# Performance work log

Hardware: AMD Instinct MI355X
Metric: run time of the kernel (lower is better)

The kernel has to match this reference:

```python
import jax, jax.numpy as jnp
import numpy as np

B, S, D, H = 8, 512, 1024, 16
DH = D // H
GAMMA = 0.1      # kl_gamma
KL_EPS = 1e-10
LN_EPS = 1e-5
SCALE = 1.0 / np.sqrt(DH).astype(np.float32)


def setup_inputs() -> dict:
    key = jax.random.key(0)
    ks = iter(jax.random.split(key, 32))
    rnd = lambda shape, s: jax.random.normal(next(ks), shape, jnp.float32) * s
    inp = {
        'title_features': rnd((B, S, D), 1.0),
        'content_features': rnd((B, S, D), 1.0),
    }
    for pre in ('t2c', 'c2t'):
        # small Q/K weights + bias 1.0 keep row-means of scores positive (log is defined)
        inp[pre + '_wq'] = rnd((D, D), 0.02); inp[pre + '_bq'] = jnp.ones((D,), jnp.float32)
        inp[pre + '_wk'] = rnd((D, D), 0.02); inp[pre + '_bk'] = jnp.ones((D,), jnp.float32)
        inp[pre + '_wv'] = rnd((D, D), 0.02); inp[pre + '_bv'] = jnp.zeros((D,), jnp.float32)
        inp[pre + '_wo'] = rnd((D, D), 0.02); inp[pre + '_bo'] = jnp.zeros((D,), jnp.float32)
    inp['gate_w'] = rnd((2 * D, D), 0.02)
    inp['gate_b'] = jnp.zeros((D,), jnp.float32)
    inp['ln_g'] = jnp.ones((D,), jnp.float32)
    inp['ln_b'] = jnpps = jnp.zeros((D,), jnp.float32)
    inp['ln_b'] = jnp.zeros((D,), jnp.float32)
    return inp


def _daa(q_in, k_in, v_in, wq, bq, wk, bk, wv, bv, wo, bo):
    """DivergenceAlignedAttention forward (eval mode, use_uniform_target=False)."""
    Bq, Sq, _ = q_in.shape
    Sk = k_in.shape[1]
    Q = (q_in @ wq + bq).reshape(Bq, Sq, H, DH)
    K = (k_in @ wk + bk).reshape(Bq, Sk, H, DH)
    V = (v_in @ wv + bv).reshape(Bq, Sk, H, DH)
    scores = jnp.einsum('bqhd,bkhd->bhqk', Q, K) * SCALE           # [B,H,Sq,Sk]
    tgt = jnp.mean(scores, axis=-1, keepdims=True)                 # row mean
    scores = scores + GAMMA * jnp.log(tgt + KL_EPS)                # fused KL term
    attn = jax.nn.softmax(scores, axis=-1)
    ctx = jnp.einsum('bhqk,bkhd->bqhd', attn, V).reshape(Bq, Sq, D)
    return ctx @ wo + bo


def _layer_norm(x, g, b):
    mu = jnp.mean(x, axis=-1, keepdims=True)
    var = jnp.mean(jnp.square(x - mu), axis=-1, keepdims=True)
    return g * (x - mu) / jnp.sqrt(var + LN_EPS) + b


def reference(title_features, content_features,
              t2c_wq, t2c_bq, t2c_wk, t2c_bk, t2c_wv, t2c_bv, t2c_wo, t2c_bo,
              c2t_wq, c2t_bq, c2t_wk, c2t_bk, c2t_wv, c2t_bv, c2t_wo, c2t_bo,
              gate_w, gate_b, ln_g, ln_b):
    t2c = _daa(content_features, title_features, title_features,
               t2c_wq, t2c_bq, t2c_wk, t2c_bk, t2c_wv, t2c_bv, t2c_wo, t2c_bo)
    c2t = _daa(title_features, content_features, content_features,
               c2t_wq, c2t_bq, c2t_wk, c2t_bk, c2t_wv, c2t_bv, c2t_wo, c2t_bo)
    gate_t = jax.nn.sigmoid(jnp.concatenate([title_features, t2c], axis=-1) @ gate_w + gate_b)
    gate_c = jax.nn.sigmoid(jnp.concatenate([content_features, c2t], axis=-1) @ gate_w + gate_b)
    fused_title = _layer_norm(gate_t * title_features + (1.0 - gate_t) * t2c, ln_g, ln_b)
    fused_content = _layer_norm(gate_c * content_features + (1.0 - gate_c) * c2t, ln_g, ln_b)
    return (fused_title, fused_content)
```

## Files before the change

### kernel.cpp

```cpp
#include <hip/hip_runtime.h>
#include <cstdint>
#include <cstddef>

typedef unsigned short ushort_t;
typedef unsigned int u32;
typedef __attribute__((ext_vector_type(8))) short bf16x8;
typedef __attribute__((ext_vector_type(4))) float f32x4;
typedef __attribute__((ext_vector_type(4))) unsigned short u16x4;

#define DEV static __device__ __forceinline__

DEV ushort_t f2bf(float f) {
  u32 x = __float_as_uint(f);
  x += 0x7fff + ((x >> 16) & 1);
  return (ushort_t)(x >> 16);
}
DEV float bf2f(ushort_t u) { return __uint_as_float(((u32)u) << 16); }

DEV void gload16(const ushort_t* g, ushort_t* l) {
  __builtin_amdgcn_global_load_lds(
      (const __attribute__((address_space(1))) void*)g,
      (__attribute__((address_space(3))) void*)l, 16, 0, 0);
}


__global__ __launch_bounds__(256) void cvt_inputs(
    const float* __restrict__ xa, const float* __restrict__ xb,
    ushort_t* __restrict__ oa, ushort_t* __restrict__ ob) {
  int i = blockIdx.x * 256 + threadIdx.x;
  f32x4 va = ((const f32x4*)xa)[i];
  f32x4 vb = ((const f32x4*)xb)[i];
  u16x4 ua, ub;
#pragma unroll
  for (int j = 0; j < 4; ++j) { ua[j] = f2bf(va[j]); ub[j] = f2bf(vb[j]); }
  ((u16x4*)oa)[i] = ua;
  ((u16x4*)ob)[i] = ub;
}

struct Src11 { const float* p[11]; };

__global__ __launch_bounds__(256) void transpose_cvt(
    Src11 srcs, ushort_t* __restrict__ WTall, ushort_t* __restrict__ WgT,
    ushort_t* __restrict__ WoBF) {
  const int z = blockIdx.z;
  if (z != 8 && blockIdx.y >= 32) return;
  const float* src = srcs.p[z];
  int tx = threadIdx.x & 31, ty = threadIdx.x >> 5;
  int n0 = blockIdx.x << 5, k0 = blockIdx.y << 5;
  if (z >= 9) {
    ushort_t* dst = WoBF + ((size_t)(z - 9) << 20);
#pragma unroll
    for (int i = 0; i < 4; ++i) {
      size_t off = (size_t)(k0 + ty + i * 8) * 1024 + n0 + tx;
      dst[off] = f2bf(src[off]);
    }
    return;
  }
  const int K = (z == 8) ? 2048 : 1024;
  ushort_t* dst = (z == 8) ? WgT : WTall + ((size_t)z << 20);
  __shared__ float t[32][33];
#pragma unroll
  for (int i = 0; i < 4; ++i)
    t[ty + i * 8][tx] = src[(size_t)(k0 + ty + i * 8) * 1024 + n0 + tx];
  __syncthreads();
#pragma unroll
  for (int i = 0; i < 4; ++i)
    dst[(size_t)(n0 + ty + i * 8) * K + k0 + tx] = f2bf(t[tx][ty + i * 8]);
}

__global__ __launch_bounds__(256) void gb2_kernel(
    const float* __restrict__ bo0, const float* __restrict__ bo1,
    const ushort_t* __restrict__ WgT, float* __restrict__ gb2) {
  const int wgl = blockIdx.x * 4 + (threadIdx.x >> 6);
  const int lane = threadIdx.x & 63;
  const int dir = wgl >> 10, n = wgl & 1023;
  const float* bo = dir ? bo1 : bo0;
  const ushort_t* wrow = WgT + ((size_t)n << 11) + 1024 + (lane << 4);
  float s = 0.f;
#pragma unroll
  for (int j = 0; j < 16; ++j) s += bo[(lane << 4) + j] * bf2f(wrow[j]);
#pragma unroll
  for (int d = 1; d < 64; d <<= 1) s += __shfl_xor(s, d, 64);
  if (lane == 0) gb2[wgl] = s;
}

__global__ __launch_bounds__(256, 3) void gemm_wp(
    const ushort_t* __restrict__ WgT, const ushort_t* __restrict__ WoBF,
    ushort_t* __restrict__ WpT) {
  __shared__ ushort_t As[128 * 64];
  __shared__ ushort_t Bs[128 * 64];
  const int tid = threadIdx.x;
  const int w = tid >> 6, lane = tid & 63;
  const int g = lane >> 4, c = lane & 15;
  const int wm = (w >> 1) << 6, wn = (w & 1) << 6;
  const int m0 = blockIdx.x << 7, n0 = blockIdx.y << 7;
  const int group = m0 >> 10;
  const int csw = (lane & 7) ^ (lane >> 3);

  f32x4 acc[4][4];
#pragma unroll
  for (int i = 0; i < 4; ++i)
#pragma unroll
    for (int j = 0; j < 4; ++j) acc[i][j] = f32x4{0.f, 0.f, 0.f, 0.f};

  for (int k0 = 0; k0 < 1024; k0 += 64) {
#pragma unroll
    for (int i = 0; i < 4; ++i) {
      const int chunk = (w << 2) + i;
      const int row = (chunk << 3) + (lane >> 3);
      gload16(WgT + ((size_t)((m0 + row) & 1023) << 11) + 1024 + k0 + (csw << 3),
              &As[(size_t)chunk << 9]);
      gload16(WoBF + ((size_t)group << 20) + ((size_t)(n0 + row) << 10) + k0 + (csw << 3),
              &Bs[(size_t)chunk << 9]);
    }
    __syncthreads();
    const int cg = c & 7;
#pragma unroll
    for (int ks = 0; ks < 2; ++ks) {
      bf16x8 af[4], bfr[4];
#pragma unroll
      for (int mi = 0; mi < 4; ++mi)
        af[mi] = *(const bf16x8*)&As[((wm + mi * 16 + c) << 6) +
                                     ((((ks << 2) | g) ^ cg) << 3)];
#pragma unroll
      for (int ni = 0; ni < 4; ++ni)
        bfr[ni] = *(const bf16x8*)&Bs[((wn + ni * 16 + c) << 6) +
                                      ((((ks << 2) | g) ^ cg) << 3)];
#pragma unroll
      for (int mi = 0; mi < 4; ++mi)
#pragma unroll
        for (int ni = 0; ni < 4; ++ni)
          acc[mi][ni] = __builtin_amdgcn_mfma_f32_16x16x32_bf16(
              af[mi], bfr[ni], acc[mi][ni], 0, 0, 0);
    }
    __syncthreads();
  }
#pragma unroll
  for (int ni = 0; ni < 4; ++ni) {
    const int n = n0 + wn + ni * 16 + c;
#pragma unroll
    for (int mi = 0; mi < 4; ++mi) {
      const int mb = m0 + wm + mi * 16 + (g << 2);
      f32x4 a = acc[mi][ni];
#pragma unroll
      for (int r = 0; r < 4; ++r)
        WpT[((size_t)group << 20) + ((size_t)((mb + r) & 1023) << 10) + n] = f2bf(a[r]);
    }
  }
}

enum { M_QKVG = 0, M_OG = 1 };
struct Bias8 { const float* p[8]; };

template <int MODE>
__global__ __launch_bounds__(256, 3) void gemm_kernel(
    const ushort_t* __restrict__ Aa, const ushort_t* __restrict__ Ab,
    const ushort_t* __restrict__ WTall, const ushort_t* __restrict__ WgT,
    const ushort_t* __restrict__ WpT, Bias8 bt, const float* __restrict__ gb2,
    ushort_t* __restrict__ outQ, ushort_t* __restrict__ gt) {
  __shared__ ushort_t As[128 * 64];
  __shared__ ushort_t Bs[128 * 64];
  const int tid = threadIdx.x;
  const int w = tid >> 6, lane = tid & 63;
  const int g = lane >> 4, c = lane & 15;
  const int wm = (w >> 1) << 6, wn = (w & 1) << 6;
  const int bid = (int)blockIdx.x;
  const int xcd = bid & 7, idx = bid >> 3;
  const int mt = (xcd << 3) + (idx & 7), nt = idx >> 3;
  const int m0 = mt << 7, n0 = nt << 7;
  const int group = m0 >> 12;
  const int nch = n0 >> 10;
  const int csw = (lane & 7) ^ (lane >> 3);

  const ushort_t* Asrc = (MODE == M_QKVG)
      ? ((group ? Ab : Aa) + ((size_t)(m0 & 4095) << 10))
      : (Aa + ((size_t)m0 << 10));

  const ushort_t* Bb;
  int bstr, bidx = -1;
  if (MODE == M_QKVG) {
    if (nch < 3) {
      bidx = group * 3 + nch;
      Bb = WTall + ((size_t)bidx << 20) + ((size_t)(n0 & 1023) << 10);
      bstr = 1024;
    } else {
      Bb = WgT + ((size_t)(n0 & 1023) << 11);
      bstr = 2048;
    }
  } else {
    if (nch == 0) {
      Bb = WTall + ((size_t)(6 + group) << 20) + ((size_t)n0 << 10);
      bstr = 1024;
    } else {
      Bb = WpT + ((size_t)group << 20) + ((size_t)(n0 & 1023) << 10);
      bstr = 1024;
    }
  }

  f32x4 acc[4][4];
#pragma unroll
  for (int i = 0; i < 4; ++i)
#pragma unroll
    for (int j = 0; j < 4; ++j) acc[i][j] = f32x4{0.f, 0.f, 0.f, 0.f};

  for (int k0 = 0; k0 < 1024; k0 += 64) {
#pragma unroll
    for (int i = 0; i < 4; ++i) {
      const int chunk = (w << 2) + i;
      const int row = (chunk << 3) + (lane >> 3);
      gload16(Asrc + ((size_t)row << 10) + k0 + (csw << 3), &As[(size_t)chunk << 9]);
      gload16(Bb + (size_t)row * bstr + k0 + (csw << 3), &Bs[(size_t)chunk << 9]);
    }
    __syncthreads();
    const int cg = c & 7;
#pragma unroll
    for (int ks = 0; ks < 2; ++ks) {
      bf16x8 af[4], bfr[4];
#pragma unroll
      for (int mi = 0; mi < 4; ++mi)
        af[mi] = *(const bf16x8*)&As[((wm + mi * 16 + c) << 6) +
                                     ((((ks << 2) | g) ^ cg) << 3)];
#pragma unroll
      for (int ni = 0; ni < 4; ++ni)
        bfr[ni] = *(const bf16x8*)&Bs[((wn + ni * 16 + c) << 6) +
                                      ((((ks << 2) | g) ^ cg) << 3)];
#pragma unroll
      for (int mi = 0; mi < 4; ++mi)
#pragma unroll
        for (int ni = 0; ni < 4; ++ni)
          acc[mi][ni] = __builtin_amdgcn_mfma_f32_16x16x32_bf16(
              af[mi], bfr[ni], acc[mi][ni], 0, 0, 0);
    }
    __syncthreads();
  }

#pragma unroll
  for (int ni = 0; ni < 4; ++ni) {
    const int n = n0 + wn + ni * 16 + c;
    const int nloc = n & 1023;
    float bv;
    if (MODE == M_QKVG)
      bv = (nch < 3) ? bt.p[bidx][nloc]
                     : bt.p[6][nloc] + gb2[(group << 10) + nloc];
    else
      bv = (nch == 0) ? bt.p[group][nloc] : 0.f;
#pragma unroll
    for (int mi = 0; mi < 4; ++mi) {
      const int mb = m0 + wm + mi * 16 + (g << 2);
      f32x4 a = acc[mi][ni];
      if (MODE == M_QKVG) {
        if (nch < 3) {
          const int mrow = mb & 4095, b = mrow >> 9, s = mrow & 511;
          const int h = nloc >> 6, d = nloc & 63;
          ushort_t* base = outQ + ((size_t)bidx << 22);
          if (bidx == 1 || bidx == 5) {
            u16x4 o;
#pragma unroll
            for (int r = 0; r < 4; ++r) o[r] = f2bf(a[r] + bv);
            *(u16x4*)&base[(((size_t)((b * 16 + h) * 64 + d)) << 9) + s] = o;
          } else {
#pragma unroll
            for (int r = 0; r < 4; ++r)
              base[(((size_t)((b * 16 + h) * 512 + s + r)) << 6) + d] = f2bf(a[r] + bv);
          }
        } else {
#pragma unroll
          for (int r = 0; r < 4; ++r)
            gt[((size_t)(mb + r) << 10) + nloc] = f2bf(a[r] + bv);
        }
      } else {
        if (nch == 0) {
#pragma unroll
          for (int r = 0; r < 4; ++r)
            outQ[((size_t)(mb + r) << 10) + nloc] = f2bf(a[r] + bv);
        } else {
#pragma unroll
          for (int r = 0; r < 4; ++r)
            gt[((size_t)(mb + r) << 10) + nloc] = f2bf(a[r]);
        }
      }
    }
  }
}

__global__ __launch_bounds__(256, 4) void attn_kernel(
    const ushort_t* __restrict__ QKV, ushort_t* __restrict__ ctx) {
  __shared__ ushort_t Ks[2][4096];
  __shared__ ushort_t Vs[2][4096];
  const int tid = threadIdx.x, w = tid >> 6, lane = tid & 63;
  const int g = lane >> 4, c = lane & 15, c7 = c & 7;
  const int bid = (int)blockIdx.x;
  const int wid = (bid & 7) * 256 + (bid >> 3);
  const int dir = wid >> 10;
  const int bh = (wid >> 3) & 127, qt = wid & 7;
  const int q0 = (qt << 6) + (w << 4);
  const int qs = dir ? 2 : 3, ks = dir ? 4 : 0, vs = dir ? 5 : 1;
  const ushort_t* Qb = QKV + ((size_t)qs << 22) + ((size_t)bh << 15);
  const ushort_t* Kb = QKV + ((size_t)ks << 22) + ((size_t)bh << 15);
  const ushort_t* Vb = QKV + ((size_t)vs << 22) + ((size_t)bh << 15);

  auto stageK = [&](int b, int kc) {
#pragma unroll
    for (int i = 0; i < 2; ++i) {
      int idx = tid + (i << 8);
      int r = idx >> 3, sl = idx & 7;
      int cs = sl ^ (r & 7);
      gload16(Kb + (((size_t)((kc << 6) + r)) << 6) + (cs << 3), &Ks[b][idx << 3]);
    }
  };
  auto stageV = [&](int b, int vc) {
#pragma unroll
    for (int i = 0; i < 2; ++i) {
      int idx = tid + (i << 8);
      int r = idx >> 3, sl = idx & 7;
      int cs = sl ^ (r & 7);
      gload16(Vb + ((size_t)r << 9) + (vc << 6) + (cs << 3), &Vs[b][idx << 3]);
    }
  };

  bf16x8 qf0 = *(const bf16x8*)&Qb[((q0 + c) << 6) + (g << 3)];
  bf16x8 qf1 = *(const bf16x8*)&Qb[((q0 + c) << 6) + 32 + (g << 3)];

  const float SC = 0.125f;
  float m = -1e30f, sum = 0.f;
  f32x4 pacc[4];
#pragma unroll
  for (int dt = 0; dt < 4; ++dt) pacc[dt] = f32x4{0.f, 0.f, 0.f, 0.f};
  const int s1 = ((g & 1) << 5) + c;
  const int s2 = s1 + 16;
  const bool hi = (g >> 1) != 0;

  stageK(0, 0);
  stageV(0, 0);
  __syncthreads();

#pragma unroll
  for (int cc = 0; cc < 8; ++cc) {
    const int buf = cc & 1;
    if (cc < 7) { stageK(buf ^ 1, cc + 1); stageV(buf ^ 1, cc + 1); }

    f32x4 st[4];
    __builtin_amdgcn_s_setprio(1);
#pragma unroll
    for (int t = 0; t < 4; ++t) {
      const ushort_t* base = &Ks[buf][((t << 4) + c) << 6];
      bf16x8 a0 = *(const bf16x8*)&base[(g ^ c7) << 3];
      bf16x8 a1 = *(const bf16x8*)&base[((4 | g) ^ c7) << 3];
      f32x4 z = {0.f, 0.f, 0.f, 0.f};
      z = __builtin_amdgcn_mfma_f32_16x16x32_bf16(a0, qf0, z, 0, 0, 0);
      z = __builtin_amdgcn_mfma_f32_16x16x32_bf16(a1, qf1, z, 0, 0, 0);
      st[t] = z;
    }
    __builtin_amdgcn_s_setprio(0);

    float mx = fmaxf(fmaxf(st[0][0], st[0][1]), fmaxf(st[0][2], st[0][3]));
#pragma unroll
    for (int t = 1; t < 4; ++t)
      mx = fmaxf(mx, fmaxf(fmaxf(st[t][0], st[t][1]), fmaxf(st[t][2], st[t][3])));
    mx = fmaxf(mx, __shfl_xor(mx, 16, 64));
    mx = fmaxf(mx, __shfl_xor(mx, 32, 64));
    const float mn = fmaxf(m, mx);
    const float scale = __expf((m - mn) * SC);
    m = mn;
    float ls = 0.f;
#pragma unroll
    for (int t = 0; t < 4; ++t)
#pragma unroll
      for (int r = 0; r < 4; ++r) {
        float p = __expf((st[t][r] - mn) * SC);
        st[t][r] = p;
        ls += p;
      }
    ls += __shfl_xor(ls, 16, 64);
    ls += __shfl_xor(ls, 32, 64);
    sum = sum * scale + ls;
#pragma unroll
    for (int dt = 0; dt < 4; ++dt)
#pragma unroll
      for (int r = 0; r < 4; ++r) pacc[dt][r] *= scale;

#pragma unroll
    for (int u = 0; u < 2; ++u) {
      u32 A0 = ((u32)f2bf(st[2 * u][1]) << 16) | f2bf(st[2 * u][0]);
      u32 A1p = ((u32)f2bf(st[2 * u][3]) << 16) | f2bf(st[2 * u][2]);
      u32 B0 = ((u32)f2bf(st[2 * u + 1][1]) << 16) | f2bf(st[2 * u + 1][0]);
      u32 B1 = ((u32)f2bf(st[2 * u + 1][3]) << 16) | f2bf(st[2 * u + 1][2]);
      u32 xA0 = (u32)__shfl((int)A0, s1, 64), xA1 = (u32)__shfl((int)A1p, s1, 64);
      u32 xB0 = (u32)__shfl((int)B0, s1, 64), xB1 = (u32)__shfl((int)B1, s1, 64);
      u32 yA0 = (u32)__shfl((int)A0, s2, 64), yA1 = (u32)__shfl((int)A1p, s2, 64);
      u32 yB0 = (u32)__shfl((int)B0, s2, 64), yB1 = (u32)__shfl((int)B1, s2, 64);
      union { bf16x8 v; u32 wd[4]; } pb;
      pb.wd[0] = hi ? xB0 : xA0;
      pb.wd[1] = hi ? xB1 : xA1;
      pb.wd[2] = hi ? yB0 : yA0;
      pb.wd[3] = hi ? yB1 : yA1;
      __builtin_amdgcn_s_setprio(1);
#pragma unroll
      for (int dt = 0; dt < 4; ++dt) {
        bf16x8 av = *(const bf16x8*)
            &Vs[buf][(((dt << 4) + c) << 6) + ((((u << 2) | g) ^ c7) << 3)];
        pacc[dt] = __builtin_amdgcn_mfma_f32_16x16x32_bf16(av, pb.v, pacc[dt], 0, 0, 0);
      }
      __builtin_amdgcn_s_setprio(0);
    }
    __syncthreads();
  }

  const float inv = 1.0f / sum;
  const int b = bh >> 4, h = bh & 15;
  size_t obase = ((size_t)dir << 22) + ((size_t)(b * 512 + q0 + c) << 10) + (h << 6);
#pragma unroll
  for (int dt = 0; dt < 4; ++dt) {
    u16x4 o;
#pragma unroll
    for (int r = 0; r < 4; ++r) o[r] = f2bf(pacc[dt][r] * inv);
    *(u16x4*)&ctx[obase + (dt << 4) + (g << 2)] = o;
  }
}

__global__ __launch_bounds__(256) void fuse_ln(
    const float* __restrict__ xt, const float* __restrict__ xc,
    const ushort_t* __restrict__ ao, const ushort_t* __restrict__ gt,
    const ushort_t* __restrict__ gp,
    const float* __restrict__ lng, const float* __restrict__ lnb,
    float* __restrict__ out) {
  const int row = blockIdx.x, dir = row >> 12, r = row & 4095;
  const float* x = (dir ? xc : xt) + ((size_t)r << 10);
  const ushort_t* a = ao + ((size_t)row << 10);
  const ushort_t* g1 = gt + ((size_t)row << 10);
  const ushort_t* g2 = gp + ((size_t)row << 10);
  float* o = out + ((size_t)row << 10);
  const int t = threadIdx.x, w = t >> 6, lane = t & 63;
  f32x4 xv = ((const f32x4*)x)[t];
  u16x4 av = ((const u16x4*)a)[t];
  u16x4 gv = ((const u16x4*)g1)[t];
  u16x4 pv = ((const u16x4*)g2)[t];
  f32x4 f;
  float sm = 0.f, sq = 0.f;
#pragma unroll
  for (int j = 0; j < 4; ++j) {
    float gate = 1.f / (1.f + __expf(-(bf2f(gv[j]) + bf2f(pv[j]))));
    float fv = gate * xv[j] + (1.f - gate) * bf2f(av[j]);
    f[j] = fv; sm += fv; sq += fv * fv;
  }
#pragma unroll
  for (int d = 1; d < 64; d <<= 1) {
    sm += __shfl_xor(sm, d, 64);
    sq += __shfl_xor(sq, d, 64);
  }
  __shared__ float ps[8];
  if (lane == 0) { ps[w] = sm; ps[4 + w] = sq; }
  __syncthreads();
  sm = ps[0] + ps[1] + ps[2] + ps[3];
  sq = ps[4] + ps[5] + ps[6] + ps[7];
  const float mu = sm * (1.f / 1024.f);
  const float var = sq * (1.f / 1024.f) - mu * mu;
  const float rstd = rsqrtf(var + 1e-5f);
  f32x4 lg = ((const f32x4*)lng)[t], lb = ((const f32x4*)lnb)[t];
  f32x4 ov;
#pragma unroll
  for (int j = 0; j < 4; ++j) ov[j] = lg[j] * (f[j] - mu) * rstd + lb[j];
  ((f32x4*)o)[t] = ov;
}

extern "C" void kernel_launch(void* const* d_in, const int* in_sizes, int n_in,
                              void* d_out, int out_size, void* d_ws, size_t ws_size,
                              hipStream_t stream) {
  (void)in_sizes; (void)n_in; (void)out_size; (void)ws_size;
  const float* title = (const float*)d_in[0];
  const float* content = (const float*)d_in[1];

  char* ws = (char*)d_ws;
  const size_t MB = 1u << 20;
  ushort_t* Xt    = (ushort_t*)(ws + 0 * MB);
  ushort_t* Xc    = (ushort_t*)(ws + 8 * MB);
  ushort_t* ctx   = (ushort_t*)(ws + 0 * MB);
  ushort_t* WTall = (ushort_t*)(ws + 16 * MB);
  ushort_t* WgT   = (ushort_t*)(ws + 32 * MB);
  ushort_t* QKV   = (ushort_t*)(ws + 36 * MB);
  ushort_t* ao    = (ushort_t*)(ws + 36 * MB);
  ushort_t* gpart = (ushort_t*)(ws + 52 * MB);
  ushort_t* gt    = (ushort_t*)(ws + 84 * MB);
  ushort_t* WoBF  = (ushort_t*)(ws + 100 * MB);
  ushort_t* WpT   = (ushort_t*)(ws + 104 * MB);
  float*    gb2   = (float*)   (ws + 108 * MB);

  cvt_inputs<<<4096, 256, 0, stream>>>(title, content, Xt, Xc);

  Src11 srcs;
  srcs.p[0] = (const float*)d_in[4];  srcs.p[1] = (const float*)d_in[6];
  srcs.p[2] = (const float*)d_in[10]; srcs.p[3] = (const float*)d_in[2];
  srcs.p[4] = (const float*)d_in[12]; srcs.p[5] = (const float*)d_in[14];
  srcs.p[6] = (const float*)d_in[8];  srcs.p[7] = (const float*)d_in[16];
  srcs.p[8] = (const float*)d_in[18];
  srcs.p[9] = (const float*)d_in[8];  srcs.p[10] = (const float*)d_in[16];
  transpose_cvt<<<dim3(32, 64, 11), 256, 0, stream>>>(srcs, WTall, WgT, WoBF);

  gb2_kernel<<<512, 256, 0, stream>>>((const float*)d_in[9], (const float*)d_in[17],
                                      WgT, gb2);
  gemm_wp<<<dim3(16, 8), 256, 0, stream>>>(WgT, WoBF, WpT);

  Bias8 bq;
  bq.p[0] = (const float*)d_in[5];  bq.p[1] = (const float*)d_in[7];
  bq.p[2] = (const float*)d_in[11]; bq.p[3] = (const float*)d_in[3];
  bq.p[4] = (const float*)d_in[13]; bq.p[5] = (const float*)d_in[15];
  bq.p[6] = (const float*)d_in[19]; bq.p[7] = nullptr;
  gemm_kernel<M_QKVG><<<2048, 256, 0, stream>>>(Xt, Xc, WTall, WgT, WpT, bq, gb2,
                                                QKV, gt);

  attn_kernel<<<2048, 256, 0, stream>>>(QKV, ctx);

  Bias8 bo;
  bo.p[0] = (const float*)d_in[9]; bo.p[1] = (const float*)d_in[17];
  for (int i = 2; i < 8; ++i) bo.p[i] = nullptr;
  gemm_kernel<M_OG><<<1024, 256, 0, stream>>>(ctx, nullptr, WTall, WgT, WpT, bo, gb2,
                                              ao, gpart);

  fuse_ln<<<8192, 256, 0, stream>>>(title, content, ao, gt, gpart,
                                    (const float*)d_in[20], (const float*)d_in[21],
                                    (float*)d_out);
}
```

Measured before the change: 224.3 us.

## Double-buffer GEMM K-loop and store Q/K row-major instead of head-major

The GEMM main loop now uses two 128x32 LDS buffers per operand and prefetches the next K slice while running MFMAs on the current one. This replaces the single-buffer load/sync/compute pattern and raises MFMA priority. Q and K projections are now written in plain [B*S, D] row-major layout rather than head-major, and the attention kernel indexes them with a 1024-element row stride. This keeps the GEMM epilogue stores contiguous, at the cost of strided per-head reads in attention and twice as many barriers per K step.

Result: slower. 245.0 us (+9.2%).

```diff
diff --git a/kernel.cpp b/kernel.cpp
--- a/kernel.cpp
+++ b/kernel.cpp
@@ -158,8 +158,8 @@
     const ushort_t* __restrict__ WTall, const ushort_t* __restrict__ WgT,
     const ushort_t* __restrict__ WpT, Bias8 bt, const float* __restrict__ gb2,
     ushort_t* __restrict__ outQ, ushort_t* __restrict__ gt) {
-  __shared__ ushort_t As[128 * 64];
-  __shared__ ushort_t Bs[128 * 64];
+  __shared__ ushort_t As[2][128 * 32];
+  __shared__ ushort_t Bs[2][128 * 32];
   const int tid = threadIdx.x;
   const int w = tid >> 6, lane = tid & 63;
   const int g = lane >> 4, c = lane & 15;
@@ -170,7 +170,6 @@
   const int m0 = mt << 7, n0 = nt << 7;
   const int group = m0 >> 12;
   const int nch = n0 >> 10;
-  const int csw = (lane & 7) ^ (lane >> 3);
 
   const ushort_t* Asrc = (MODE == M_QKVG)
       ? ((group ? Ab : Aa) + ((size_t)(m0 & 4095) << 10))
@@ -197,40 +196,48 @@
     }
   }
 
+  auto stage = [&](int bf_, int k0) {
+#pragma unroll
+    for (int j = 0; j < 2; ++j) {
+      const int blkc = (w << 1) + j;
+      const int row = (blkc << 4) + (lane >> 2);
+      const int cs = (lane & 3) ^ ((row >> 1) & 3);
+      gload16(Asrc + ((size_t)row << 10) + k0 + (cs << 3), &As[bf_][blkc << 9]);
+      gload16(Bb + (size_t)row * bstr + k0 + (cs << 3), &Bs[bf_][blkc << 9]);
+    }
+  };
+
   f32x4 acc[4][4];
 #pragma unroll
   for (int i = 0; i < 4; ++i)
 #pragma unroll
     for (int j = 0; j < 4; ++j) acc[i][j] = f32x4{0.f, 0.f, 0.f, 0.f};
 
-  for (int k0 = 0; k0 < 1024; k0 += 64) {
-#pragma unroll
-    for (int i = 0; i < 4; ++i) {
-      const int chunk = (w << 2) + i;
-      const int row = (chunk << 3) + (lane >> 3);
-      gload16(Asrc + ((size_t)row << 10) + k0 + (csw << 3), &As[(size_t)chunk << 9]);
-      gload16(Bb + (size_t)row * bstr + k0 + (csw << 3), &Bs[(size_t)chunk << 9]);
-    }
-    __syncthreads();
-    const int cg = c & 7;
-#pragma unroll
-    for (int ks = 0; ks < 2; ++ks) {
-      bf16x8 af[4], bfr[4];
-#pragma unroll
-      for (int mi = 0; mi < 4; ++mi)
-        af[mi] = *(const bf16x8*)&As[((wm + mi * 16 + c) << 6) +
-                                     ((((ks << 2) | g) ^ cg) << 3)];
+  stage(0, 0);
+  __syncthreads();
+#pragma unroll 2
+  for (int t = 0; t < 32; ++t) {
+    const int buf = t & 1;
+    if (t < 31) stage(buf ^ 1, (t + 1) << 5);
+    bf16x8 af[4], bfr[4];
+#pragma unroll
+    for (int mi = 0; mi < 4; ++mi) {
+      const int row = wm + mi * 16 + c;
+      af[mi] = *(const bf16x8*)&As[buf][(row << 5) + ((g ^ ((row >> 1) & 3)) << 3)];
+    }
+#pragma unroll
+    for (int ni = 0; ni < 4; ++ni) {
+      const int row = wn + ni * 16 + c;
+      bfr[ni] = *(const bf16x8*)&Bs[buf][(row << 5) + ((g ^ ((row >> 1) & 3)) << 3)];
+    }
+    __builtin_amdgcn_s_setprio(1);
+#pragma unroll
+    for (int mi = 0; mi < 4; ++mi)
 #pragma unroll
       for (int ni = 0; ni < 4; ++ni)
-        bfr[ni] = *(const bf16x8*)&Bs[((wn + ni * 16 + c) << 6) +
-                                      ((((ks << 2) | g) ^ cg) << 3)];
-#pragma unroll
-      for (int mi = 0; mi < 4; ++mi)
-#pragma unroll
-        for (int ni = 0; ni < 4; ++ni)
-          acc[mi][ni] = __builtin_amdgcn_mfma_f32_16x16x32_bf16(
-              af[mi], bfr[ni], acc[mi][ni], 0, 0, 0);
-    }
+        acc[mi][ni] = __builtin_amdgcn_mfma_f32_16x16x32_bf16(
+            af[mi], bfr[ni], acc[mi][ni], 0, 0, 0);
+    __builtin_amdgcn_s_setprio(0);
     __syncthreads();
   }
 
@@ -250,10 +257,11 @@
       f32x4 a = acc[mi][ni];
       if (MODE == M_QKVG) {
         if (nch < 3) {
-          const int mrow = mb & 4095, b = mrow >> 9, s = mrow & 511;
-          const int h = nloc >> 6, d = nloc & 63;
+          const int mrow = mb & 4095;
           ushort_t* base = outQ + ((size_t)bidx << 22);
           if (bidx == 1 || bidx == 5) {
+            const int b = mrow >> 9, s = mrow & 511;
+            const int h = nloc >> 6, d = nloc & 63;
             u16x4 o;
 #pragma unroll
             for (int r = 0; r < 4; ++r) o[r] = f2bf(a[r] + bv);
@@ -261,7 +269,7 @@
           } else {
 #pragma unroll
             for (int r = 0; r < 4; ++r)
-              base[(((size_t)((b * 16 + h) * 512 + s + r)) << 6) + d] = f2bf(a[r] + bv);
+              base[((size_t)(mrow + r) << 10) + nloc] = f2bf(a[r] + bv);
           }
         } else {
 #pragma unroll
@@ -293,33 +301,34 @@
   const int wid = (bid & 7) * 256 + (bid >> 3);
   const int dir = wid >> 10;
   const int bh = (wid >> 3) & 127, qt = wid & 7;
+  const int b = bh >> 4, h = bh & 15;
   const int q0 = (qt << 6) + (w << 4);
   const int qs = dir ? 2 : 3, ks = dir ? 4 : 0, vs = dir ? 5 : 1;
-  const ushort_t* Qb = QKV + ((size_t)qs << 22) + ((size_t)bh << 15);
-  const ushort_t* Kb = QKV + ((size_t)ks << 22) + ((size_t)bh << 15);
+  const ushort_t* Qb = QKV + ((size_t)qs << 22) + (((size_t)b << 9) << 10) + (h << 6);
+  const ushort_t* Kb = QKV + ((size_t)ks << 22) + (((size_t)b << 9) << 10) + (h << 6);
   const ushort_t* Vb = QKV + ((size_t)vs << 22) + ((size_t)bh << 15);
 
-  auto stageK = [&](int b, int kc) {
+  auto stageK = [&](int bb, int kc) {
 #pragma unroll
     for (int i = 0; i < 2; ++i) {
       int idx = tid + (i << 8);
       int r = idx >> 3, sl = idx & 7;
       int cs = sl ^ (r & 7);
-      gload16(Kb + (((size_t)((kc << 6) + r)) << 6) + (cs << 3), &Ks[b][idx << 3]);
+      gload16(Kb + ((size_t)((kc << 6) + r) << 10) + (cs << 3), &Ks[bb][idx << 3]);
     }
   };
-  auto stageV = [&](int b, int vc) {
+  auto stageV = [&](int bb, int vc) {
 #pragma unroll
     for (int i = 0; i < 2; ++i) {
       int idx = tid + (i << 8);
       int r = idx >> 3, sl = idx & 7;
       int cs = sl ^ (r & 7);
-      gload16(Vb + ((size_t)r << 9) + (vc << 6) + (cs << 3), &Vs[b][idx << 3]);
+      gload16(Vb + ((size_t)r << 9) + (vc << 6) + (cs << 3), &Vs[bb][idx << 3]);
     }
   };
 
-  bf16x8 qf0 = *(const bf16x8*)&Qb[((q0 + c) << 6) + (g << 3)];
-  bf16x8 qf1 = *(const bf16x8*)&Qb[((q0 + c) << 6) + 32 + (g << 3)];
+  bf16x8 qf0 = *(const bf16x8*)&Qb[((size_t)(q0 + c) << 10) + (g << 3)];
+  bf16x8 qf1 = *(const bf16x8*)&Qb[((size_t)(q0 + c) << 10) + 32 + (g << 3)];
 
   const float SC = 0.125f;
   float m = -1e30f, sum = 0.f;
@@ -407,7 +416,6 @@
   }
 
   const float inv = 1.0f / sum;
-  const int b = bh >> 4, h = bh & 15;
   size_t obase = ((size_t)dir << 22) + ((size_t)(b * 512 + q0 + c) << 10) + (h << 6);
 #pragma unroll
   for (int dt = 0; dt < 4; ++dt) {
```

## Stage GEMM epilogue through LDS for coalesced row-major Q/K stores

Applied to the files above, without the earlier changes.

The GEMM epilogue now writes the bias-added bf16 tile into shared memory and then stores it to global memory as 16-byte row-major vectors. Before, Q and K were scattered as 2-byte writes into a head-split [b,h,s,d] layout. Q and K therefore now stay in plain [B*S, D] row-major layout, and the attention kernel reads them with a 1024-element row stride instead of 64. The aim is to remove the uncoalesced narrow stores, at the cost of an extra LDS round trip, a barrier, and strided K/Q loads in attention.

Result: no change. 225.4 us (+0.5%).

```diff
diff --git a/kernel.cpp b/kernel.cpp
--- a/kernel.cpp
+++ b/kernel.cpp
@@ -158,8 +158,9 @@
     const ushort_t* __restrict__ WTall, const ushort_t* __restrict__ WgT,
     const ushort_t* __restrict__ WpT, Bias8 bt, const float* __restrict__ gb2,
     ushort_t* __restrict__ outQ, ushort_t* __restrict__ gt) {
-  __shared__ ushort_t As[128 * 64];
-  __shared__ ushort_t Bs[128 * 64];
+  __shared__ ushort_t smem[16384];
+  ushort_t* As = smem;
+  ushort_t* Bs = smem + 8192;
   const int tid = threadIdx.x;
   const int w = tid >> 6, lane = tid & 63;
   const int g = lane >> 4, c = lane & 15;
@@ -234,51 +235,63 @@
     __syncthreads();
   }
 
-#pragma unroll
-  for (int ni = 0; ni < 4; ++ni) {
-    const int n = n0 + wn + ni * 16 + c;
-    const int nloc = n & 1023;
-    float bv;
-    if (MODE == M_QKVG)
-      bv = (nch < 3) ? bt.p[bidx][nloc]
-                     : bt.p[6][nloc] + gb2[(group << 10) + nloc];
-    else
-      bv = (nch == 0) ? bt.p[group][nloc] : 0.f;
-#pragma unroll
-    for (int mi = 0; mi < 4; ++mi) {
-      const int mb = m0 + wm + mi * 16 + (g << 2);
-      f32x4 a = acc[mi][ni];
-      if (MODE == M_QKVG) {
-        if (nch < 3) {
-          const int mrow = mb & 4095, b = mrow >> 9, s = mrow & 511;
-          const int h = nloc >> 6, d = nloc & 63;
-          ushort_t* base = outQ + ((size_t)bidx << 22);
-          if (bidx == 1 || bidx == 5) {
-            u16x4 o;
-#pragma unroll
-            for (int r = 0; r < 4; ++r) o[r] = f2bf(a[r] + bv);
-            *(u16x4*)&base[(((size_t)((b * 16 + h) * 64 + d)) << 9) + s] = o;
-          } else {
-#pragma unroll
-            for (int r = 0; r < 4; ++r)
-              base[(((size_t)((b * 16 + h) * 512 + s + r)) << 6) + d] = f2bf(a[r] + bv);
-          }
-        } else {
-#pragma unroll
-          for (int r = 0; r < 4; ++r)
-            gt[((size_t)(mb + r) << 10) + nloc] = f2bf(a[r] + bv);
-        }
-      } else {
-        if (nch == 0) {
-#pragma unroll
-          for (int r = 0; r < 4; ++r)
-            outQ[((size_t)(mb + r) << 10) + nloc] = f2bf(a[r] + bv);
-        } else {
-#pragma unroll
-          for (int r = 0; r < 4; ++r)
-            gt[((size_t)(mb + r) << 10) + nloc] = f2bf(a[r]);
-        }
+  const bool vt_path = (MODE == M_QKVG) && (nch < 3) && (bidx == 1 || bidx == 5);
+  if (vt_path) {
+#pragma unroll
+    for (int ni = 0; ni < 4; ++ni) {
+      const int nloc = (n0 + wn + ni * 16 + c) & 1023;
+      const float bv = bt.p[bidx][nloc];
+      const int h = nloc >> 6, d = nloc & 63;
+#pragma unroll
+      for (int mi = 0; mi < 4; ++mi) {
+        const int mrow = (m0 + wm + mi * 16 + (g << 2)) & 4095;
+        const int b = mrow >> 9, s = mrow & 511;
+        f32x4 a = acc[mi][ni];
+        u16x4 o;
+#pragma unroll
+        for (int r = 0; r < 4; ++r) o[r] = f2bf(a[r] + bv);
+        *(u16x4*)&outQ[((size_t)bidx << 22) +
+                       (((size_t)((b * 16 + h) * 64 + d)) << 9) + s] = o;
       }
+    }
+  } else {
+#pragma unroll
+    for (int ni = 0; ni < 4; ++ni) {
+      const int col = wn + ni * 16 + c;
+      const int nloc = (n0 + col) & 1023;
+      float bv;
+      if (MODE == M_QKVG)
+        bv = (nch < 3) ? bt.p[bidx][nloc]
+                       : bt.p[6][nloc] + gb2[(group << 10) + nloc];
+      else
+        bv = (nch == 0) ? bt.p[group][nloc] : 0.f;
+#pragma unroll
+      for (int mi = 0; mi < 4; ++mi) {
+        const int rowb = wm + mi * 16 + (g << 2);
+        f32x4 a = acc[mi][ni];
+#pragma unroll
+        for (int r = 0; r < 4; ++r)
+          smem[((rowb + r) << 7) + col] = f2bf(a[r] + bv);
+      }
+    }
+    __syncthreads();
+    const int lr = tid >> 4;
+    const int lc = (tid & 15) << 3;
+    ushort_t* obase;
+    size_t rbase;
+    if (MODE == M_QKVG) {
+      if (nch < 3) { obase = outQ + ((size_t)bidx << 22); rbase = (size_t)(m0 & 4095); }
+      else         { obase = gt;                          rbase = (size_t)m0; }
+    } else {
+      if (nch == 0) { obase = outQ; rbase = (size_t)m0; }
+      else          { obase = gt;   rbase = (size_t)m0; }
+    }
+    const int ncol = (n0 & 1023) + lc;
+#pragma unroll
+    for (int j = 0; j < 8; ++j) {
+      const int row = (j << 4) + lr;
+      bf16x8 v = *(const bf16x8*)&smem[(row << 7) + lc];
+      *(bf16x8*)&obase[((rbase + row) << 10) + ncol] = v;
     }
   }
 }
@@ -293,33 +306,34 @@
   const int wid = (bid & 7) * 256 + (bid >> 3);
   const int dir = wid >> 10;
   const int bh = (wid >> 3) & 127, qt = wid & 7;
+  const int b = bh >> 4, h = bh & 15;
   const int q0 = (qt << 6) + (w << 4);
   const int qs = dir ? 2 : 3, ks = dir ? 4 : 0, vs = dir ? 5 : 1;
-  const ushort_t* Qb = QKV + ((size_t)qs << 22) + ((size_t)bh << 15);
-  const ushort_t* Kb = QKV + ((size_t)ks << 22) + ((size_t)bh << 15);
+  const ushort_t* Qb = QKV + ((size_t)qs << 22) + (((size_t)b << 9) << 10) + (h << 6);
+  const ushort_t* Kb = QKV + ((size_t)ks << 22) + (((size_t)b << 9) << 10) + (h << 6);
   const ushort_t* Vb = QKV + ((size_t)vs << 22) + ((size_t)bh << 15);
 
-  auto stageK = [&](int b, int kc) {
+  auto stageK = [&](int bb, int kc) {
 #pragma unroll
     for (int i = 0; i < 2; ++i) {
       int idx = tid + (i << 8);
       int r = idx >> 3, sl = idx & 7;
       int cs = sl ^ (r & 7);
-      gload16(Kb + (((size_t)((kc << 6) + r)) << 6) + (cs << 3), &Ks[b][idx << 3]);
+      gload16(Kb + ((size_t)((kc << 6) + r) << 10) + (cs << 3), &Ks[bb][idx << 3]);
     }
   };
-  auto stageV = [&](int b, int vc) {
+  auto stageV = [&](int bb, int vc) {
 #pragma unroll
     for (int i = 0; i < 2; ++i) {
       int idx = tid + (i << 8);
       int r = idx >> 3, sl = idx & 7;
       int cs = sl ^ (r & 7);
-      gload16(Vb + ((size_t)r << 9) + (vc << 6) + (cs << 3), &Vs[b][idx << 3]);
+      gload16(Vb + ((size_t)r << 9) + (vc << 6) + (cs << 3), &Vs[bb][idx << 3]);
     }
   };
 
-  bf16x8 qf0 = *(const bf16x8*)&Qb[((q0 + c) << 6) + (g << 3)];
-  bf16x8 qf1 = *(const bf16x8*)&Qb[((q0 + c) << 6) + 32 + (g << 3)];
+  bf16x8 qf0 = *(const bf16x8*)&Qb[((size_t)(q0 + c) << 10) + (g << 3)];
+  bf16x8 qf1 = *(const bf16x8*)&Qb[((size_t)(q0 + c) << 10) + 32 + (g << 3)];
 
   const float SC = 0.125f;
   float m = -1e30f, sum = 0.f;
@@ -407,7 +421,6 @@
   }
 
   const float inv = 1.0f / sum;
-  const int b = bh >> 4, h = bh & 15;
   size_t obase = ((size_t)dir << 22) + ((size_t)(b * 512 + q0 + c) << 10) + (h << 6);
 #pragma unroll
   for (int dt = 0; dt < 4; ++dt) {
```
